# Optimization experiments

Measured on AMD Instinct MI355X. Metric: run time of the kernel, lower is better.

The kernel has to match this reference:

```python
import jax, jax.numpy as jnp
import numpy as np

B, S, H = 32, 255, 1024
BS, WD, O = 120, 20, 10
HSZ = 2 * (BS + 1) + WD  # 262


def setup_inputs() -> dict:
    key = jax.random.key(0)
    ks = jax.random.split(key, 9)
    inv = lambda *d: 1.0 / np.sqrt(d[0])
    return {
        "state": jax.random.normal(ks[0], (B, S, H), jnp.float32),
        "head_w": jax.random.normal(ks[1], (H, BS), jnp.float32) * inv(H),
        "head_b": jax.random.normal(ks[2], (BS,), jnp.float32) * 0.02,
        "tail_w": jax.random.normal(ks[3], (H, BS), jnp.float32) * inv(H),
        "tail_b": jax.random.normal(ks[4], (BS,), jnp.float32) * 0.02,
        "U": jax.random.normal(ks[5], (O, BS, BS), jnp.float32) * inv(BS),
        "width_table": jax.random.normal(ks[6], (256, WD), jnp.float32).at[0].set(0.0),  # padding_idx=0
        "cls_w": jax.random.normal(ks[7], (O, HSZ), jnp.float32) * inv(HSZ),
        "cls_b": jax.random.normal(ks[8], (O,), jnp.float32) * 0.02,
    }


def _leaky_relu(x):
    return jnp.where(x >= 0, x, 0.01 * x)  # torch LeakyReLU default slope


def reference(state, head_w, head_b, tail_w, tail_b, U, width_table, cls_w, cls_b):
    b, s, _ = state.shape
    bs = head_w.shape[1]
    # head/tail MLPs (dropout is identity in eval)
    h = _leaky_relu(state @ head_w + head_b)  # (b, s, bs)
    t = _leaky_relu(state @ tail_w + tail_b)  # (b, s, bs)

    # bilinear term
    scores1 = jnp.einsum('bxi,oij,byj->bxyo', h, U, t)  # (b, s, s, O)

    # append bias-ones feature
    ones = jnp.ones((b, s, 1), h.dtype)
    h1 = jnp.concatenate([h, ones], axis=-1)  # (b, s, bs+1)
    t1 = jnp.concatenate([t, ones], axis=-1)

    # span-width embedding: pos[x, y] = y - x + 1, clamped to 0 for y < x
    pos = jnp.arange(s)[None, :] - jnp.arange(s)[:, None] + 1
    pos = pos * (pos > 0)
    wemb = width_table[pos]  # (s, s, WD)

    # cls(concat(h1_x, t1_y, wemb_xy)) decomposed into three small projections
    # + broadcast-add; mathematically identical to materializing affined_cat.
    Wh = cls_w[:, :bs + 1]              # (O, bs+1)
    Wt = cls_w[:, bs + 1:2 * (bs + 1)]  # (O, bs+1)
    Ww = cls_w[:, 2 * (bs + 1):]        # (O, WD)
    scores2 = (jnp.einsum('bxi,oi->bxo', h1, Wh)[:, :, None, :]
               + jnp.einsum('byi,oi->byo', t1, Wt)[:, None, :, :]
               + jnp.einsum('xyw,ow->xyo', wemb, Ww)[None]
               + cls_b)
    return scores1 + scores2
```

## Files before the change

kernel.cpp:

```cpp
#include <hip/hip_runtime.h>
#include <hip/hip_bf16.h>

using f32x4 = __attribute__((ext_vector_type(4))) float;
using s16x8 = __attribute__((ext_vector_type(8))) short;
using s16x4 = __attribute__((ext_vector_type(4))) short;

constexpr int S = 255, RTOT = 32 * 255;

__device__ inline unsigned short f2bf(float x) {
    __hip_bfloat16 b = __float2bfloat16(x);
    return __builtin_bit_cast(unsigned short, b);
}
__device__ inline float bf2f(unsigned short u) {
    unsigned int t = ((unsigned int)u) << 16;
    return __builtin_bit_cast(float, t);
}
__device__ inline f32x4 mfma16(s16x8 a, s16x8 b, f32x4 c) {
    return __builtin_amdgcn_mfma_f32_16x16x32_bf16(a, b, c, 0, 0, 0);
}
__device__ inline void gload16(const unsigned short* g, unsigned short* l) {
    __builtin_amdgcn_global_load_lds(
        (const __attribute__((address_space(1))) void*)g,
        (__attribute__((address_space(3))) void*)l, 16, 0, 0);
}


__global__ __launch_bounds__(256) void convert_k(
    const float* __restrict__ head_w, const float* __restrict__ tail_w,
    const float* __restrict__ U, const float* __restrict__ wtab,
    const float* __restrict__ cls_w,
    unsigned short* __restrict__ WP, unsigned short* __restrict__ Ut,
    float* __restrict__ tblp)
{
    int gid = blockIdx.x * 256 + threadIdx.x;
    if (gid < 262144) {
        int e = gid & 7, kcp = (gid >> 3) & 7, n = (gid >> 6) & 255, ks = gid >> 14;
        int kc = kcp ^ (n & 7);
        int k = ks * 64 + kc * 8 + e;
        float v;
        if (n < 128) v = (n < 120) ? head_w[k * 120 + n] : 0.f;
        else { int nn = n - 128; v = (nn < 120) ? tail_w[k * 120 + nn] : 0.f; }
        WP[gid] = f2bf(v);
    } else if (gid < 262144 + 163840) {
        int idx = gid - 262144;
        int j = idx & 127, i2 = (idx >> 7) & 127, o = idx >> 14;
        float v = (i2 < 120 && j < 120) ? U[((size_t)o * 120 + i2) * 120 + j] : 0.f;
        int ph = (((i2 >> 3) ^ (j & 7)) << 3) | (i2 & 7);
        Ut[(size_t)o * 16384 + (size_t)j * 128 + ph] = f2bf(v);
    } else {
        int id = gid - 262144 - 163840;
        if (id < 2560) {
            int p = id / 10, o = id - (id / 10) * 10;
            float s = 0.f;
            #pragma unroll
            for (int wq = 0; wq < 20; ++wq)
                s += wtab[p * 20 + wq] * cls_w[o * 262 + 242 + wq];
            tblp[p * 12 + o] = s;
        }
    }
}

__global__ __launch_bounds__(256) void ht_mfma(
    const float* __restrict__ state, const unsigned short* __restrict__ WP,
    const float* __restrict__ head_b, const float* __restrict__ tail_b,
    const float* __restrict__ cls_w, const float* __restrict__ cls_b,
    unsigned short* __restrict__ hbuf, unsigned short* __restrict__ tbuf,
    float* __restrict__ hwp, float* __restrict__ twp)
{
    __shared__ unsigned short Ss[2][32 * 64];
    __shared__ unsigned short Ws[2][256 * 64];
    const int r0 = blockIdx.x * 32;
    const int tid = threadIdx.x;
    const int w = tid >> 6, lane = tid & 63;
    const int l16 = lane & 15, kq = lane >> 4;
    const int srow = tid >> 3, skc = tid & 7;
    const float* sp = &state[(size_t)(r0 + srow) * 1024 + skc * 8];

    f32x4 acc[4][2];
    #pragma unroll
    for (int fn = 0; fn < 4; ++fn)
        #pragma unroll
        for (int fr = 0; fr < 2; ++fr) acc[fn][fr] = (f32x4){0.f, 0.f, 0.f, 0.f};

    #pragma unroll
    for (int j = 0; j < 8; ++j) {
        int off = (w * 8 + j) * 512;
        gload16(WP + off + lane * 8, &Ws[0][off]);
    }
    {
        f32x4 a0 = *(const f32x4*)sp;
        f32x4 a1 = *(const f32x4*)(sp + 4);
        s16x8 pk;
        #pragma unroll
        for (int e = 0; e < 4; ++e) { pk[e] = (short)f2bf(a0[e]); pk[e + 4] = (short)f2bf(a1[e]); }
        *(s16x8*)((char*)&Ss[0][0] + srow * 128 + ((skc * 16) ^ ((srow & 7) << 4))) = pk;
    }
    __syncthreads();

    for (int it = 0; it < 16; ++it) {
        const int cur = it & 1;
        f32x4 a0, a1;
        if (it < 15) {
            #pragma unroll
            for (int j = 0; j < 8; ++j) {
                int off = (w * 8 + j) * 512;
                gload16(WP + (it + 1) * 16384 + off + lane * 8, &Ws[cur ^ 1][off]);
            }
            a0 = *(const f32x4*)(sp + (it + 1) * 64);
            a1 = *(const f32x4*)(sp + (it + 1) * 64 + 4);
        }
        const char* SsB = (const char*)&Ss[cur][0];
        const char* WsB = (const char*)&Ws[cur][0];
        s16x8 bf[2][2];
        #pragma unroll
        for (int fr = 0; fr < 2; ++fr) {
            int rr = fr * 16 + l16;
            #pragma unroll
            for (int ks = 0; ks < 2; ++ks)
                bf[fr][ks] = *(const s16x8*)(SsB + rr * 128 + ((ks * 64 + kq * 16) ^ ((rr & 7) << 4)));
        }
        #pragma unroll
        for (int fn = 0; fn < 4; ++fn) {
            int n = w * 64 + fn * 16 + l16;
            #pragma unroll
            for (int ks = 0; ks < 2; ++ks) {
                s16x8 af = *(const s16x8*)(WsB + n * 128 + ((ks * 64 + kq * 16) ^ ((n & 7) << 4)));
                #pragma unroll
                for (int fr = 0; fr < 2; ++fr)
                    acc[fn][fr] = mfma16(af, bf[fr][ks], acc[fn][fr]);
            }
        }
        if (it < 15) {
            s16x8 pk;
            #pragma unroll
            for (int e = 0; e < 4; ++e) { pk[e] = (short)f2bf(a0[e]); pk[e + 4] = (short)f2bf(a1[e]); }
            *(s16x8*)((char*)&Ss[cur ^ 1][0] + srow * 128 + ((skc * 16) ^ ((srow & 7) << 4))) = pk;
        }
        __syncthreads();
    }

    unsigned short* Hl = &Ws[0][0];
    unsigned short* Tl = &Ws[1][0];
    #pragma unroll
    for (int fn = 0; fn < 4; ++fn) {
        const int n0 = w * 64 + fn * 16 + kq * 4;
        const int isT = n0 >= 128;
        const int c0 = n0 & 127;
        const int g = c0 >> 3, sub = (kq & 1) * 4;
        const float* bp = isT ? tail_b : head_b;
        #pragma unroll
        for (int fr = 0; fr < 2; ++fr) {
            const int rloc = fr * 16 + l16;
            const int r = r0 + rloc;
            s16x4 pk;
            #pragma unroll
            for (int e = 0; e < 4; ++e) {
                float bv = (c0 + e < 120) ? bp[c0 + e] : 0.f;
                float z = acc[fn][fr][e] + bv;
                z = (z >= 0.f) ? z : 0.01f * z;
                pk[e] = (short)f2bf(z);
            }
            if (isT) {
                int bq = r / 255, x = r - bq * 255;
                *(s16x4*)&tbuf[((size_t)bq * 256 + x) * 128 + ((g ^ (x & 7)) << 3) + sub] = pk;
                *(s16x4*)&Tl[rloc * 128 + c0] = pk;
            } else {
                *(s16x4*)&hbuf[(size_t)r * 128 + ((g ^ (r & 7)) << 3) + sub] = pk;
                *(s16x4*)&Hl[rloc * 128 + c0] = pk;
            }
        }
    }
    __syncthreads();

    float* Wl = (float*)&Ws[0][4096];
    for (int idx = tid; idx < 2430; idx += 256) {
        if (idx < 2420) {
            int which = idx / 1210, rem = idx - which * 1210;
            int o = rem / 121, i = rem - o * 121;
            Wl[idx] = cls_w[o * 262 + which * 121 + i];
        } else Wl[idx] = cls_b[idx - 2420];
    }
    __syncthreads();
    for (int d = tid; d < 640; d += 256) {
        int which = d / 320, rem = d - which * 320;
        int rr = rem / 10, o = rem - rr * 10;
        const unsigned short* row = (which ? Tl : Hl) + rr * 128;
        const float* wp2 = &Wl[which * 1210 + o * 121];
        float s = 0.f;
        #pragma unroll
        for (int c = 0; c < 15; ++c) {
            s16x8 v = *(const s16x8*)&row[c * 8];
            #pragma unroll
            for (int e = 0; e < 8; ++e)
                s += bf2f((unsigned short)v[e]) * wp2[c * 8 + e];
        }
        s += wp2[120];
        int gr = r0 + rr;
        if (!which) hwp[(size_t)gr * 12 + o] = s + Wl[2420 + o];
        else        twp[(size_t)gr * 12 + o] = s;
    }
}

__global__ __launch_bounds__(256) void hU_mfma(
    const unsigned short* __restrict__ hbuf, const unsigned short* __restrict__ Ut,
    unsigned short* __restrict__ hU)
{
    __shared__ unsigned short Hs[128 * 128];
    __shared__ unsigned short Us[128 * 128];
    const int r0 = blockIdx.x * 128;
    const int o = blockIdx.y;
    const int tid = threadIdx.x;
    const int w = tid >> 6, lane = tid & 63;
    const int l16 = lane & 15, kq = lane >> 4;
    const char* HsB = (const char*)Hs;
    const char* UsB = (const char*)Us;

    #pragma unroll
    for (int j = 0; j < 8; ++j) {
        int off = (w * 8 + j) * 512;
        gload16(&hbuf[(size_t)r0 * 128 + off + lane * 8], &Hs[off]);
        gload16(&Ut[(size_t)o * 16384 + off + lane * 8], &Us[off]);
    }
    __syncthreads();

    f32x4 acc[2][8];
    #pragma unroll
    for (int a = 0; a < 2; ++a)
        #pragma unroll
        for (int b2 = 0; b2 < 8; ++b2) acc[a][b2] = (f32x4){0.f, 0.f, 0.f, 0.f};

    #pragma unroll
    for (int ks = 0; ks < 4; ++ks) {
        int kb = ks * 64 + kq * 16;
        s16x8 bf[2];
        #pragma unroll
        for (int fr = 0; fr < 2; ++fr) {
            int row = w * 32 + fr * 16 + l16;
            bf[fr] = *(const s16x8*)(HsB + row * 256 + (kb ^ ((row & 7) << 4)));
        }
        #pragma unroll
        for (int fj = 0; fj < 8; ++fj) {
            int j = fj * 16 + l16;
            s16x8 af = *(const s16x8*)(UsB + j * 256 + (kb ^ ((j & 7) << 4)));
            #pragma unroll
            for (int fr = 0; fr < 2; ++fr)
                acc[fr][fj] = mfma16(af, bf[fr], acc[fr][fj]);
        }
    }

    #pragma unroll
    for (int fr = 0; fr < 2; ++fr) {
        int r = r0 + w * 32 + fr * 16 + l16;
        if (r < RTOT) {
            int bq = r / 255, x = r - bq * 255;
            int m = x * 12 + o;
            size_t rowbase = ((size_t)bq * 3072 + m) * 128;
            int key = m & 7, sub = (kq & 1) * 4;
            #pragma unroll
            for (int fj = 0; fj < 8; ++fj) {
                int g = fj * 2 + (kq >> 1);
                s16x4 pk;
                #pragma unroll
                for (int e = 0; e < 4; ++e) pk[e] = (short)f2bf(acc[fr][fj][e]);
                *(s16x4*)&hU[rowbase + ((g ^ key) << 3) + sub] = pk;
            }
        }
    }
}

__global__ __launch_bounds__(512) void main_mfma(
    const unsigned short* __restrict__ hU, const unsigned short* __restrict__ tbuf,
    const float* __restrict__ hwp, const float* __restrict__ twp,
    const float* __restrict__ tblp, float* __restrict__ out)
{
    __shared__ unsigned short Bs[256 * 128];
    __shared__ unsigned short As[2][128 * 128];
    const int mg = blockIdx.x, b = blockIdx.y;
    const int tid = threadIdx.x;
    const int w = tid >> 6, lane = tid & 63;
    const int l16 = lane & 15, kq = lane >> 4;
    const int wm = w >> 2, wy = w & 3;
    const size_t hUbase = (size_t)b * 3072 * 128;
    const size_t tbase = (size_t)b * 256 * 128;

    #pragma unroll
    for (int j = 0; j < 8; ++j) {
        int off = (w * 8 + j) * 512;
        gload16(&tbuf[tbase + off + lane * 8], &Bs[off]);
    }
    {
        const size_t a0 = hUbase + (size_t)(mg * 3 * 128) * 128;
        #pragma unroll
        for (int j = 0; j < 4; ++j) {
            int off = (w * 4 + j) * 512;
            gload16(&hU[a0 + off + lane * 8], &As[0][off]);
        }
    }
    __syncthreads();

    s16x8 bfr[4][4];
    #pragma unroll
    for (int ks = 0; ks < 4; ++ks)
        #pragma unroll
        for (int fy = 0; fy < 4; ++fy) {
            int row = wy * 64 + fy * 16 + l16;
            bfr[ks][fy] = *(const s16x8*)((const char*)Bs + row * 256 +
                           ((ks * 64 + kq * 16) ^ ((row & 7) << 4)));
        }

    for (int i = 0; i < 3; ++i) {
        const int m0 = (mg * 3 + i) * 128;
        if (i < 2) {
            const size_t an = hUbase + (size_t)(m0 + 128) * 128;
            #pragma unroll
            for (int j = 0; j < 4; ++j) {
                int off = (w * 4 + j) * 512;
                gload16(&hU[an + off + lane * 8], &As[(i + 1) & 1][off]);
            }
        }
        const char* AsB = (const char*)&As[i & 1][0];
        f32x4 acc[4][4];
        #pragma unroll
        for (int fm = 0; fm < 4; ++fm)
            #pragma unroll
            for (int fy = 0; fy < 4; ++fy) acc[fm][fy] = (f32x4){0.f, 0.f, 0.f, 0.f};

        #pragma unroll
        for (int ks = 0; ks < 4; ++ks) {
            s16x8 af[4];
            #pragma unroll
            for (int fm = 0; fm < 4; ++fm) {
                int row = wm * 64 + fm * 16 + l16;
                af[fm] = *(const s16x8*)(AsB + row * 256 +
                          ((ks * 64 + kq * 16) ^ ((row & 7) << 4)));
            }
            #pragma unroll
            for (int fm = 0; fm < 4; ++fm)
                #pragma unroll
                for (int fy = 0; fy < 4; ++fy)
                    acc[fm][fy] = mfma16(af[fm], bfr[ks][fy], acc[fm][fy]);
        }

        __syncthreads();

        #pragma unroll
        for (int fm = 0; fm < 4; ++fm) {
            const int ml = m0 + wm * 64 + fm * 16 + kq * 4;
            if (ml < 3060) {
                const int x = ml / 12, o0 = ml % 12;
                const int rx = b * 255 + x;
                f32x4 hv = *(const f32x4*)&hwp[(size_t)rx * 12 + o0];
                #pragma unroll
                for (int fy = 0; fy < 4; ++fy) {
                    const int y = wy * 64 + fy * 16 + l16;
                    if (y < 255) {
                        const int ry = b * 255 + y;
                        f32x4 tv = *(const f32x4*)&twp[(size_t)ry * 12 + o0];
                        int p = y - x + 1; if (p < 0) p = 0;
                        f32x4 wv = *(const f32x4*)&tblp[p * 12 + o0];
                        float* op = &out[((size_t)rx * 255 + y) * 10 + o0];
                        if (o0 < 8) {
                            float v[4];
                            #pragma unroll
                            for (int e = 0; e < 4; ++e)
                                v[e] = acc[fm][fy][e] + hv[e] + tv[e] + wv[e];
                            __builtin_memcpy(op, v, 16);
                        } else {
                            float v[2];
                            v[0] = acc[fm][fy][0] + hv[0] + tv[0] + wv[0];
                            v[1] = acc[fm][fy][1] + hv[1] + tv[1] + wv[1];
                            __builtin_memcpy(op, v, 8);
                        }
                    }
                }
            }
        }
    }
}

extern "C" void kernel_launch(void* const* d_in, const int* in_sizes, int n_in,
                              void* d_out, int out_size, void* d_ws, size_t ws_size,
                              hipStream_t stream)
{
    (void)in_sizes; (void)n_in; (void)out_size; (void)ws_size;
    const float* state  = (const float*)d_in[0];
    const float* head_w = (const float*)d_in[1];
    const float* head_b = (const float*)d_in[2];
    const float* tail_w = (const float*)d_in[3];
    const float* tail_b = (const float*)d_in[4];
    const float* U      = (const float*)d_in[5];
    const float* wtab   = (const float*)d_in[6];
    const float* cls_w  = (const float*)d_in[7];
    const float* cls_b  = (const float*)d_in[8];
    float* out = (float*)d_out;

    unsigned short* u16 = (unsigned short*)d_ws;
    unsigned short* hbuf = u16;
    unsigned short* tbuf = hbuf + 1044480;
    unsigned short* hUb  = tbuf + 1048576;
    unsigned short* WP   = hUb + 12582912;
    unsigned short* Ut   = WP + 262144;
    float* hwp  = (float*)(Ut + 163840);
    float* twp  = hwp + 97920;
    float* tblp = twp + 97920;

    hipLaunchKernelGGL(convert_k, dim3(1674), dim3(256), 0, stream,
                       head_w, tail_w, U, wtab, cls_w, WP, Ut, tblp);
    hipLaunchKernelGGL(ht_mfma, dim3(255), dim3(256), 0, stream,
                       state, WP, head_b, tail_b, cls_w, cls_b,
                       hbuf, tbuf, hwp, twp);
    hipLaunchKernelGGL(hU_mfma, dim3(64, 10), dim3(256), 0, stream,
                       hbuf, Ut, hUb);
    hipLaunchKernelGGL(main_mfma, dim3(8, 32), dim3(512), 0, stream,
                       hUb, tbuf, hwp, twp, tblp, out);
}
```

Before: 89.50 us.

## Fuse hU bilinear projection into head/tail kernel and remap main grid order

Removes the separate hU_mfma kernel. The h·U product is now computed inside ht_mfma, reading h tiles from LDS and U fragments straight from global memory, so the hbuf round trip and one launch go away. The LDS copies of h/t are XOR-swizzled to match, and Ut is stored unswizzled. main_mfma remaps block IDs so that blocks sharing a batch are spread across XCDs. In exchange, ht_mfma does more serial work per block (10 output classes looped over 255 blocks), and the uncached U loads repeat across blocks.

```diff
diff --git a/kernel.cpp b/kernel.cpp
--- a/kernel.cpp
+++ b/kernel.cpp
@@ -5,7 +5,7 @@
 using s16x8 = __attribute__((ext_vector_type(8))) short;
 using s16x4 = __attribute__((ext_vector_type(4))) short;
 
-constexpr int S = 255, RTOT = 32 * 255;
+constexpr int RTOT = 32 * 255;
 
 __device__ inline unsigned short f2bf(float x) {
     __hip_bfloat16 b = __float2bfloat16(x);
@@ -45,8 +45,7 @@
         int idx = gid - 262144;
         int j = idx & 127, i2 = (idx >> 7) & 127, o = idx >> 14;
         float v = (i2 < 120 && j < 120) ? U[((size_t)o * 120 + i2) * 120 + j] : 0.f;
-        int ph = (((i2 >> 3) ^ (j & 7)) << 3) | (i2 & 7);
-        Ut[(size_t)o * 16384 + (size_t)j * 128 + ph] = f2bf(v);
+        Ut[(size_t)o * 16384 + (size_t)j * 128 + i2] = f2bf(v);
     } else {
         int id = gid - 262144 - 163840;
         if (id < 2560) {
@@ -62,9 +61,10 @@
 
 __global__ __launch_bounds__(256) void ht_mfma(
     const float* __restrict__ state, const unsigned short* __restrict__ WP,
+    const unsigned short* __restrict__ Ut,
     const float* __restrict__ head_b, const float* __restrict__ tail_b,
     const float* __restrict__ cls_w, const float* __restrict__ cls_b,
-    unsigned short* __restrict__ hbuf, unsigned short* __restrict__ tbuf,
+    unsigned short* __restrict__ tbuf, unsigned short* __restrict__ hUb,
     float* __restrict__ hwp, float* __restrict__ twp)
 {
     __shared__ unsigned short Ss[2][32 * 64];
@@ -146,8 +146,9 @@
         const int n0 = w * 64 + fn * 16 + kq * 4;
         const int isT = n0 >= 128;
         const int c0 = n0 & 127;
-        const int g = c0 >> 3, sub = (kq & 1) * 4;
+        const int g = c0 >> 3, sub = c0 & 7;
         const float* bp = isT ? tail_b : head_b;
+        unsigned short* dstl = isT ? Tl : Hl;
         #pragma unroll
         for (int fr = 0; fr < 2; ++fr) {
             const int rloc = fr * 16 + l16;
@@ -160,13 +161,10 @@
                 z = (z >= 0.f) ? z : 0.01f * z;
                 pk[e] = (short)f2bf(z);
             }
+            *(s16x4*)&dstl[rloc * 128 + ((g ^ (rloc & 7)) << 3) + sub] = pk;
             if (isT) {
                 int bq = r / 255, x = r - bq * 255;
                 *(s16x4*)&tbuf[((size_t)bq * 256 + x) * 128 + ((g ^ (x & 7)) << 3) + sub] = pk;
-                *(s16x4*)&Tl[rloc * 128 + c0] = pk;
-            } else {
-                *(s16x4*)&hbuf[(size_t)r * 128 + ((g ^ (r & 7)) << 3) + sub] = pk;
-                *(s16x4*)&Hl[rloc * 128 + c0] = pk;
             }
         }
     }
@@ -181,6 +179,59 @@
         } else Wl[idx] = cls_b[idx - 2420];
     }
     __syncthreads();
+
+    {
+        s16x8 bh[2][4];
+        #pragma unroll
+        for (int rf = 0; rf < 2; ++rf) {
+            int rr = rf * 16 + l16;
+            #pragma unroll
+            for (int ks = 0; ks < 4; ++ks)
+                bh[rf][ks] = *(const s16x8*)((const char*)Hl + rr * 256 +
+                              ((ks * 64 + kq * 16) ^ ((rr & 7) << 4)));
+        }
+        size_t rbase[2]; int x4[2];
+        #pragma unroll
+        for (int rf = 0; rf < 2; ++rf) {
+            int gr = r0 + rf * 16 + l16;
+            int bq = gr / 255, x = gr - bq * 255;
+            rbase[rf] = ((size_t)bq * 3072 + x * 12) * 128;
+            x4[rf] = x * 4;
+        }
+        for (int o = 0; o < 10; ++o) {
+            f32x4 acc1[2][2];
+            #pragma unroll
+            for (int jf = 0; jf < 2; ++jf)
+                #pragma unroll
+                for (int rf = 0; rf < 2; ++rf) acc1[jf][rf] = (f32x4){0.f, 0.f, 0.f, 0.f};
+            #pragma unroll
+            for (int ks = 0; ks < 4; ++ks) {
+                #pragma unroll
+                for (int jf = 0; jf < 2; ++jf) {
+                    int j = w * 32 + jf * 16 + l16;
+                    s16x8 af = *(const s16x8*)&Ut[(size_t)o * 16384 +
+                                (size_t)j * 128 + ks * 32 + kq * 8];
+                    #pragma unroll
+                    for (int rf = 0; rf < 2; ++rf)
+                        acc1[jf][rf] = mfma16(af, bh[rf][ks], acc1[jf][rf]);
+                }
+            }
+            #pragma unroll
+            for (int jf = 0; jf < 2; ++jf) {
+                int j0 = w * 32 + jf * 16 + kq * 4;
+                int g = j0 >> 3, sub = j0 & 7;
+                #pragma unroll
+                for (int rf = 0; rf < 2; ++rf) {
+                    int key = (x4[rf] + o) & 7;
+                    s16x4 pk;
+                    #pragma unroll
+                    for (int e = 0; e < 4; ++e) pk[e] = (short)f2bf(acc1[jf][rf][e]);
+                    *(s16x4*)&hUb[rbase[rf] + (size_t)o * 128 + ((g ^ key) << 3) + sub] = pk;
+                }
+            }
+        }
+    }
+
     for (int d = tid; d < 640; d += 256) {
         int which = d / 320, rem = d - which * 320;
         int rr = rem / 10, o = rem - rr * 10;
@@ -189,7 +240,7 @@
         float s = 0.f;
         #pragma unroll
         for (int c = 0; c < 15; ++c) {
-            s16x8 v = *(const s16x8*)&row[c * 8];
+            s16x8 v = *(const s16x8*)&row[(c ^ (rr & 7)) << 3];
             #pragma unroll
             for (int e = 0; e < 8; ++e)
                 s += bf2f((unsigned short)v[e]) * wp2[c * 8 + e];
@@ -198,73 +249,6 @@
         int gr = r0 + rr;
         if (!which) hwp[(size_t)gr * 12 + o] = s + Wl[2420 + o];
         else        twp[(size_t)gr * 12 + o] = s;
-    }
-}
-
-__global__ __launch_bounds__(256) void hU_mfma(
-    const unsigned short* __restrict__ hbuf, const unsigned short* __restrict__ Ut,
-    unsigned short* __restrict__ hU)
-{
-    __shared__ unsigned short Hs[128 * 128];
-    __shared__ unsigned short Us[128 * 128];
-    const int r0 = blockIdx.x * 128;
-    const int o = blockIdx.y;
-    const int tid = threadIdx.x;
-    const int w = tid >> 6, lane = tid & 63;
-    const int l16 = lane & 15, kq = lane >> 4;
-    const char* HsB = (const char*)Hs;
-    const char* UsB = (const char*)Us;
-
-    #pragma unroll
-    for (int j = 0; j < 8; ++j) {
-        int off = (w * 8 + j) * 512;
-        gload16(&hbuf[(size_t)r0 * 128 + off + lane * 8], &Hs[off]);
-        gload16(&Ut[(size_t)o * 16384 + off + lane * 8], &Us[off]);
-    }
-    __syncthreads();
-
-    f32x4 acc[2][8];
-    #pragma unroll
-    for (int a = 0; a < 2; ++a)
-        #pragma unroll
-        for (int b2 = 0; b2 < 8; ++b2) acc[a][b2] = (f32x4){0.f, 0.f, 0.f, 0.f};
-
-    #pragma unroll
-    for (int ks = 0; ks < 4; ++ks) {
-        int kb = ks * 64 + kq * 16;
-        s16x8 bf[2];
-        #pragma unroll
-        for (int fr = 0; fr < 2; ++fr) {
-            int row = w * 32 + fr * 16 + l16;
-            bf[fr] = *(const s16x8*)(HsB + row * 256 + (kb ^ ((row & 7) << 4)));
-        }
-        #pragma unroll
-        for (int fj = 0; fj < 8; ++fj) {
-            int j = fj * 16 + l16;
-            s16x8 af = *(const s16x8*)(UsB + j * 256 + (kb ^ ((j & 7) << 4)));
-            #pragma unroll
-            for (int fr = 0; fr < 2; ++fr)
-                acc[fr][fj] = mfma16(af, bf[fr], acc[fr][fj]);
-        }
-    }
-
-    #pragma unroll
-    for (int fr = 0; fr < 2; ++fr) {
-        int r = r0 + w * 32 + fr * 16 + l16;
-        if (r < RTOT) {
-            int bq = r / 255, x = r - bq * 255;
-            int m = x * 12 + o;
-            size_t rowbase = ((size_t)bq * 3072 + m) * 128;
-            int key = m & 7, sub = (kq & 1) * 4;
-            #pragma unroll
-            for (int fj = 0; fj < 8; ++fj) {
-                int g = fj * 2 + (kq >> 1);
-                s16x4 pk;
-                #pragma unroll
-                for (int e = 0; e < 4; ++e) pk[e] = (short)f2bf(acc[fr][fj][e]);
-                *(s16x4*)&hU[rowbase + ((g ^ key) << 3) + sub] = pk;
-            }
-        }
     }
 }
 
@@ -275,7 +259,9 @@
 {
     __shared__ unsigned short Bs[256 * 128];
     __shared__ unsigned short As[2][128 * 128];
-    const int mg = blockIdx.x, b = blockIdx.y;
+    const int wgid = blockIdx.x + (blockIdx.y << 3);
+    const int virt = (wgid & 7) * 32 + (wgid >> 3);
+    const int b = virt >> 3, mg = virt & 7;
     const int tid = threadIdx.x;
     const int w = tid >> 6, lane = tid & 63;
     const int l16 = lane & 15, kq = lane >> 4;
@@ -395,8 +381,7 @@
     float* out = (float*)d_out;
 
     unsigned short* u16 = (unsigned short*)d_ws;
-    unsigned short* hbuf = u16;
-    unsigned short* tbuf = hbuf + 1044480;
+    unsigned short* tbuf = u16;
     unsigned short* hUb  = tbuf + 1048576;
     unsigned short* WP   = hUb + 12582912;
     unsigned short* Ut   = WP + 262144;
@@ -407,10 +392,8 @@
     hipLaunchKernelGGL(convert_k, dim3(1674), dim3(256), 0, stream,
                        head_w, tail_w, U, wtab, cls_w, WP, Ut, tblp);
     hipLaunchKernelGGL(ht_mfma, dim3(255), dim3(256), 0, stream,
-                       state, WP, head_b, tail_b, cls_w, cls_b,
-                       hbuf, tbuf, hwp, twp);
-    hipLaunchKernelGGL(hU_mfma, dim3(64, 10), dim3(256), 0, stream,
-                       hbuf, Ut, hUb);
+                       state, WP, Ut, head_b, tail_b, cls_w, cls_b,
+                       tbuf, hUb, hwp, twp);
     hipLaunchKernelGGL(main_mfma, dim3(8, 32), dim3(512), 0, stream,
                        hUb, tbuf, hwp, twp, tblp, out);
 }
```

Result: faster. 87.05 us (-2.7%).
